# Kernel optimization log

Measured on AMD Instinct MI355X. Metric: run time of the kernel, lower is better.

The kernel has to match this reference:

```python
import jax, jax.numpy as jnp
import numpy as np
from jax import lax

BS = 16; NG = 512; L = 2048; HOP = 512; ZD = 128; HD = 512
FS = L // 2 + 1
TAR = (NG - 1) * HOP + L  # 263680, matches int((NG+3)/4*L)
PPC = 5; PPK = 65
LOG10 = float(np.log(10.0))

def _hann_periodic(n):
    return (0.5 * (1.0 - np.cos(2.0 * np.pi * np.arange(n) / n))).astype(np.float32)

# filter window: fftshift(hann_window(L)) (torch periodic hann)
_FW = jnp.asarray(np.fft.fftshift(_hann_periodic(L)))
# OLA windows with edge correction (first/last grain half set to center value 1.0)
_w = _hann_periodic(L)
_ow = np.tile(_w[None, :], (NG, 1))
_ow[0, : L // 2] = _w[L // 2]
_ow[-1, L // 2 :] = _w[L // 2]
_OLA_W = jnp.asarray(_ow)  # [NG, L]
# overlap-add scatter indices and divisor (fold(unfold(ones)))
_IDX = jnp.asarray((np.arange(NG)[:, None] * HOP + np.arange(L)[None, :]).reshape(-1))
_DIV = jnp.zeros((TAR,), jnp.float32).at[_IDX].add(1.0)


def setup_inputs() -> dict:
    key = jax.random.key(0)
    ks = jax.random.split(key, 8)
    s = 0.02
    d = {}
    d["z"] = jax.random.normal(ks[0], (BS * NG, ZD), jnp.float32)
    d["w0"] = jax.random.normal(ks[1], (ZD, HD), jnp.float32) * s
    d["b0"] = jnp.zeros((HD,), jnp.float32)
    d["g0"] = jnp.ones((HD,), jnp.float32)
    d["be0"] = jnp.zeros((HD,), jnp.float32)
    d["w1"] = jax.random.normal(ks[2], (HD, HD), jnp.float32) * s
    d["b1"] = jnp.zeros((HD,), jnp.float32)
    d["g1"] = jnp.ones((HD,), jnp.float32)
    d["be1"] = jnp.zeros((HD,), jnp.float32)
    d["w2"] = jax.random.normal(ks[3], (HD, HD), jnp.float32) * s
    d["b2"] = jnp.zeros((HD,), jnp.float32)
    d["g2"] = jnp.ones((HD,), jnp.float32)
    d["be2"] = jnp.zeros((HD,), jnp.float32)
    d["w3"] = jax.random.normal(ks[4], (HD, FS), jnp.float32) * s
    d["b3"] = jnp.zeros((FS,), jnp.float32)
    d["pp_w"] = jax.random.normal(ks[5], (1, PPC, PPK), jnp.float32) * s
    d["pp_b"] = jnp.zeros((1,), jnp.float32)
    d["noise"] = jax.random.uniform(ks[6], (BS * NG, L), jnp.float32) * 2.0 - 1.0
    return d


def _lin_bn_lrelu(x, w, b, g, be):
    h = x @ w + b
    m = h.mean(0)
    v = jnp.mean((h - m) ** 2, 0)  # biased var (train-mode BatchNorm1d)
    h = (h - m) * lax.rsqrt(v + 1e-5) * g + be
    return jnp.where(h >= 0, h, 0.2 * h)  # LeakyReLU(0.2)


def reference(z, w0, b0, g0, be0, w1, b1, g1, be1, w2, b2, g2, be2, w3, b3, pp_w, pp_b, noise):
    # decoder MLP -> filter coefficients
    h = _lin_bn_lrelu(z, w0, b0, g0, be0)
    h = _lin_bn_lrelu(h, w1, b1, g1, be1)
    h = _lin_bn_lrelu(h, w2, b2, g2, be2)
    fc = h @ w3 + b3  # [BS*NG, FS]
    fc = 2.0 * jax.nn.sigmoid(fc) ** LOG10 + 1e-7  # mod_sigmoid
    # noise filtering in spectral domain
    ir = jnp.fft.irfft(fc.astype(jnp.complex64), n=L, axis=-1).astype(jnp.float32)
    ir = jnp.fft.fftshift(ir * _FW[None, :], axes=-1)
    audio = jnp.fft.irfft(jnp.fft.rfft(noise, axis=-1) * jnp.fft.rfft(ir, axis=-1), n=L, axis=-1).astype(jnp.float32)
    # per-grain windowing + overlap-add (nn.Fold equivalent scatter-add)
    audio = audio.reshape(BS, NG, L) * _OLA_W[None]
    audio_sum = jnp.zeros((BS, TAR), jnp.float32).at[:, _IDX].add(audio.reshape(BS, -1))
    audio_sum = audio_sum / _DIV  # normalize_ola
    # post-processing conv (PPC replicated channels -> 1) + softsign
    x = jnp.broadcast_to(audio_sum[:, None, :], (BS, PPC, TAR))
    y = lax.conv_general_dilated(x, pp_w, (1,), [(PPK // 2, PPK // 2)], dimension_numbers=("NCH", "OIH", "NCH"))
    y = y[:, 0, :] + pp_b[0]
    return y / (1.0 + jnp.abs(y))
```

## Files before the change

### kernel.cpp

```cpp
#include <hip/hip_runtime.h>
#include <hip/hip_bf16.h>
#include <math.h>

#define TARLEN 263680
#define POWEXP 2.302585092994046f
#define PC(i) ((i) + ((i) >> 3))

typedef __attribute__((ext_vector_type(8))) short bf16x8;
typedef __attribute__((ext_vector_type(8))) ushort u16x8;
typedef __attribute__((ext_vector_type(4))) float f32x4;
typedef __attribute__((ext_vector_type(2))) float pf2;

__device__ __forceinline__ void gload16(const void* g, void* l) {
    __builtin_amdgcn_global_load_lds((const __attribute__((address_space(1))) void*)g,
                                     (__attribute__((address_space(3))) void*)l, 16, 0, 0);
}

__device__ __forceinline__ float bf16f(ushort u) {
    union { uint u; float f; } v; v.u = (uint)u << 16; return v.f;
}
__device__ __forceinline__ ushort fbf16(float x) {
    __hip_bfloat16 h = __float2bfloat16(x);
    return *reinterpret_cast<ushort*>(&h);
}

__device__ __forceinline__ float vsin_rev(float rev) {
    float r; asm("v_sin_f32 %0, %1" : "=v"(r) : "v"(rev)); return r;
}
__device__ __forceinline__ float vcos_rev(float rev) {
    float r; asm("v_cos_f32 %0, %1" : "=v"(r) : "v"(rev)); return r;
}

__device__ __forceinline__ pf2 cmulp(pf2 a, float c, float s) {
    return a * c + a.yx * (pf2){-s, s};
}

__global__ __launch_bounds__(512) void gemm8(
    const ushort* __restrict__ A, const ushort* __restrict__ Bt,
    const float* __restrict__ bias, ushort* __restrict__ C,
    int K, float* __restrict__ ps, float* __restrict__ pq)
{
    __shared__ ushort As[3][4096];
    __shared__ ushort Bs[3][4096];
    __shared__ float sred[8][2][16];
    __shared__ float qred[8][2][16];
    const int tid = threadIdx.x;
    const int lane = tid & 63;
    const int wid = tid >> 6;
    const int nwg = gridDim.x * gridDim.y;
    const int bid = blockIdx.y * gridDim.x + blockIdx.x;
    const int q8 = nwg >> 3;
    const int swzb = (bid & 7) * q8 + (bid >> 3);
    const int bx = swzb % gridDim.x;
    const int by = swzb / gridDim.x;
    const int m0 = by * 128;
    const int n0 = bx * 128;
    const int NT = K >> 5;

    f32x4 acc[4][2];
#pragma unroll
    for (int m = 0; m < 4; ++m)
#pragma unroll
        for (int n = 0; n < 2; ++n)
            acc[m][n] = (f32x4){0.f, 0.f, 0.f, 0.f};

    const int srow = tid >> 2;
    const int scol = (((tid & 3) ^ ((tid >> 3) & 3)) << 3);

    auto stage = [&](int t, int buf) {
        const int k0 = t << 5;
        gload16(A + (size_t)(m0 + srow) * K + k0 + scol, &As[buf][tid * 8]);
        gload16(Bt + (size_t)(n0 + srow) * K + k0 + scol, &Bs[buf][tid * 8]);
    };

    const int lr = lane & 15;
    const int sw8 = (((lane >> 4) ^ ((lane >> 1) & 3)) << 3);
    const int wm0 = (wid >> 2) * 64;
    const int wn0 = (wid & 3) * 32;

    stage(0, 0);
    stage(1, 1);
    for (int t = 0; t < NT; ++t) {
        const int cur = t % 3;
        if (t + 2 < NT) {
            asm volatile("s_waitcnt vmcnt(2)" ::: "memory");
            __builtin_amdgcn_s_barrier();
            stage(t + 2, (t + 2) % 3);
        } else {
            asm volatile("s_waitcnt vmcnt(0)" ::: "memory");
            __builtin_amdgcn_s_barrier();
        }
        const ushort* as = As[cur];
        const ushort* bs = Bs[cur];
        bf16x8 af[4], bfv[2];
#pragma unroll
        for (int m = 0; m < 4; ++m)
            af[m] = *reinterpret_cast<const bf16x8*>(&as[(wm0 + m * 16 + lr) * 32 + sw8]);
#pragma unroll
        for (int n = 0; n < 2; ++n)
            bfv[n] = *reinterpret_cast<const bf16x8*>(&bs[(wn0 + n * 16 + lr) * 32 + sw8]);
#pragma unroll
        for (int m = 0; m < 4; ++m)
#pragma unroll
            for (int n = 0; n < 2; ++n)
                acc[m][n] = __builtin_amdgcn_mfma_f32_16x16x32_bf16(af[m], bfv[n], acc[m][n], 0, 0, 0);
    }
    __syncthreads();

    const int cr = (lane >> 4) << 2;
    const int cc = lane & 15;
    float sacc[2] = {0.f, 0.f}, qacc[2] = {0.f, 0.f};
#pragma unroll
    for (int m = 0; m < 4; ++m) {
#pragma unroll
        for (int n = 0; n < 2; ++n) {
            int gcol = n0 + wn0 + n * 16 + cc;
            float bv = bias[gcol];
            int grow = m0 + wm0 + m * 16 + cr;
#pragma unroll
            for (int j = 0; j < 4; ++j) {
                float v = acc[m][n][j] + bv;
                sacc[n] += v;
                qacc[n] += v * v;
                C[(size_t)(grow + j) * 512 + gcol] = fbf16(v);
            }
        }
    }
#pragma unroll
    for (int n = 0; n < 2; ++n) {
        float s = sacc[n], q = qacc[n];
        s += __shfl_xor(s, 16); q += __shfl_xor(q, 16);
        s += __shfl_xor(s, 32); q += __shfl_xor(q, 32);
        if (lane < 16) { sred[wid][n][lane] = s; qred[wid][n][lane] = q; }
    }
    __syncthreads();
    if (tid < 128) {
        int wn_ = tid >> 5, n_ = (tid >> 4) & 1, cc_ = tid & 15;
        float s = sred[wn_][n_][cc_] + sred[4 + wn_][n_][cc_];
        float q = qred[wn_][n_][cc_] + qred[4 + wn_][n_][cc_];
        int col = n0 + wn_ * 32 + n_ * 16 + cc_;
        ps[(size_t)by * 512 + col] = s;
        pq[(size_t)by * 512 + col] = q;
    }
}

template<int EPI>
__global__ __launch_bounds__(512) void gemm8n(
    const ushort* __restrict__ H, const ushort* __restrict__ Bt,
    const float* __restrict__ bias,
    const float* __restrict__ psIn, const float* __restrict__ pqIn,
    const float* __restrict__ gamma, const float* __restrict__ beta,
    ushort* __restrict__ C, int K, int Nvalid, int ldc,
    float* __restrict__ psOut, float* __restrict__ pqOut)
{
    __shared__ ushort As[3][4096];
    __shared__ ushort Bs[3][4096];
    __shared__ uint sab[512];
    __shared__ float sred[8][2][16];
    __shared__ float qred[8][2][16];
    const int tid = threadIdx.x;
    const int lane = tid & 63;
    const int wid = tid >> 6;
    const int nwg = gridDim.x * gridDim.y;
    const int bid = blockIdx.y * gridDim.x + blockIdx.x;
    const int q8 = nwg >> 3;
    const int swzb = (bid & 7) * q8 + (bid >> 3);
    const int bx = swzb % gridDim.x;
    const int by = swzb / gridDim.x;
    const int m0 = by * 128;
    const int n0 = bx * 128;
    const int NT = K >> 5;

    {
        int c = tid;
        float s = 0.f, q = 0.f;
#pragma unroll 8
        for (int rg = 0; rg < 64; ++rg) { s += psIn[rg * 512 + c]; q += pqIn[rg * 512 + c]; }
        float m = s * (1.f / 8192.f);
        float v = q * (1.f / 8192.f) - m * m;
        float a = rsqrtf(v + 1e-5f) * gamma[c];
        float b = beta[c] - m * a;
        sab[c] = (uint)fbf16(a) | ((uint)fbf16(b) << 16);
    }

    f32x4 acc[4][2];
#pragma unroll
    for (int m = 0; m < 4; ++m)
#pragma unroll
        for (int n = 0; n < 2; ++n)
            acc[m][n] = (f32x4){0.f, 0.f, 0.f, 0.f};

    const int srow = tid >> 2;
    const int scol = (((tid & 3) ^ ((tid >> 3) & 3)) << 3);
    const int lr = lane & 15;
    const int sw8 = (((lane >> 4) ^ ((lane >> 1) & 3)) << 3);
    const int wm0 = (wid >> 2) * 64;
    const int wn0 = (wid & 3) * 32;

    const size_t arow = (size_t)(m0 + srow) * K + scol;
    const size_t brow = (size_t)(n0 + srow) * K + scol;

    auto stageB = [&](int t, int buf) {
        gload16(Bt + brow + (t << 5), &Bs[buf][tid * 8]);
    };
    auto loadA = [&](int t, u16x8& dst) {
        dst = *reinterpret_cast<const u16x8*>(H + arow + (t << 5));
    };

    __syncthreads();

    u16x8 a0, a1;
    stageB(0, 0); loadA(0, a0);
    stageB(1, 1); loadA(1, a1);

    auto iter = [&](int t, u16x8& ar) {
        const int cur = t % 3;
        if (t + 2 < NT) asm volatile("s_waitcnt vmcnt(2)" ::: "memory");
        else            asm volatile("s_waitcnt vmcnt(0)" ::: "memory");
        {
            const uint* pk = &sab[(t << 5) + scol];
            u16x8 o;
#pragma unroll
            for (int j = 0; j < 8; ++j) {
                uint w = pk[j];
                float a = bf16f((ushort)(w & 0xffffu));
                float b = bf16f((ushort)(w >> 16));
                float y = fmaf(bf16f(ar[j]), a, b);
                o[j] = fbf16(y >= 0.f ? y : 0.2f * y);
            }
            *reinterpret_cast<u16x8*>(&As[cur][tid * 8]) = o;
        }
        asm volatile("s_waitcnt lgkmcnt(0)" ::: "memory");
        __builtin_amdgcn_s_barrier();
        if (t + 2 < NT) { stageB(t + 2, (t + 2) % 3); loadA(t + 2, ar); }
        const ushort* as = As[cur];
        const ushort* bs = Bs[cur];
        bf16x8 af[4], bfv[2];
#pragma unroll
        for (int m = 0; m < 4; ++m)
            af[m] = *reinterpret_cast<const bf16x8*>(&as[(wm0 + m * 16 + lr) * 32 + sw8]);
#pragma unroll
        for (int n = 0; n < 2; ++n)
            bfv[n] = *reinterpret_cast<const bf16x8*>(&bs[(wn0 + n * 16 + lr) * 32 + sw8]);
#pragma unroll
        for (int m = 0; m < 4; ++m)
#pragma unroll
            for (int n = 0; n < 2; ++n)
                acc[m][n] = __builtin_amdgcn_mfma_f32_16x16x32_bf16(af[m], bfv[n], acc[m][n], 0, 0, 0);
    };

    for (int t = 0; t < NT; t += 2) { iter(t, a0); iter(t + 1, a1); }
    __syncthreads();

    const int cr = (lane >> 4) << 2;
    const int cc = lane & 15;
    float sacc[2] = {0.f, 0.f}, qacc[2] = {0.f, 0.f};
#pragma unroll
    for (int m = 0; m < 4; ++m) {
#pragma unroll
        for (int n = 0; n < 2; ++n) {
            int gcol = n0 + wn0 + n * 16 + cc;
            if (EPI == 0 || gcol < Nvalid) {
                float bv = bias[gcol];
                int grow = m0 + wm0 + m * 16 + cr;
#pragma unroll
                for (int j = 0; j < 4; ++j) {
                    float v = acc[m][n][j] + bv;
                    if (EPI == 1) {
                        float sg = 1.f / (1.f + __expf(-v));
                        v = 2.f * __expf(POWEXP * __logf(sg)) + 1e-7f;
                    } else {
                        sacc[n] += v;
                        qacc[n] += v * v;
                    }
                    C[(size_t)(grow + j) * ldc + gcol] = fbf16(v);
                }
            }
        }
    }
    if (EPI == 0) {
#pragma unroll
        for (int n = 0; n < 2; ++n) {
            float s = sacc[n], q = qacc[n];
            s += __shfl_xor(s, 16); q += __shfl_xor(q, 16);
            s += __shfl_xor(s, 32); q += __shfl_xor(q, 32);
            if (lane < 16) { sred[wid][n][lane] = s; qred[wid][n][lane] = q; }
        }
        __syncthreads();
        if (tid < 128) {
            int wn_ = tid >> 5, n_ = (tid >> 4) & 1, cc_ = tid & 15;
            float s = sred[wn_][n_][cc_] + sred[4 + wn_][n_][cc_];
            float q = qred[wn_][n_][cc_] + qred[4 + wn_][n_][cc_];
            int col = n0 + wn_ * 32 + n_ * 16 + cc_;
            psOut[(size_t)by * 512 + col] = s;
            pqOut[(size_t)by * 512 + col] = q;
        }
    }
}

__global__ __launch_bounds__(256) void prep_inputs(
    const float* __restrict__ w0, const float* __restrict__ w1,
    const float* __restrict__ w2, const float* __restrict__ w3,
    const float* __restrict__ z,
    ushort* __restrict__ B0, ushort* __restrict__ B1,
    ushort* __restrict__ B2, ushort* __restrict__ B3,
    ushort* __restrict__ A)
{
    if (blockIdx.z == 4) {
        int bid = blockIdx.y * gridDim.x + blockIdx.x;
        if (bid >= 512) return;
        int idx = (bid * 256 + threadIdx.x) << 3;
        float4 a = *reinterpret_cast<const float4*>(&z[idx]);
        float4 b = *reinterpret_cast<const float4*>(&z[idx + 4]);
        float x[8] = {a.x, a.y, a.z, a.w, b.x, b.y, b.z, b.w};
        u16x8 o;
#pragma unroll
        for (int j = 0; j < 8; ++j) o[j] = fbf16(x[j]);
        *reinterpret_cast<u16x8*>(&A[idx]) = o;
        return;
    }
    const float* w; ushort* Bt; int K, N, GX, GY;
    switch (blockIdx.z) {
        case 0: w = w0; Bt = B0; K = 128; N = 512;  GX = 4;  GY = 16; break;
        case 1: w = w1; Bt = B1; K = 512; N = 512;  GX = 16; GY = 16; break;
        case 2: w = w2; Bt = B2; K = 512; N = 512;  GX = 16; GY = 16; break;
        default:w = w3; Bt = B3; K = 512; N = 1025; GX = 16; GY = 36; break;
    }
    if ((int)blockIdx.x >= GX || (int)blockIdx.y >= GY) return;
    __shared__ float tile[32][33];
    int k0 = blockIdx.x * 32, n0 = blockIdx.y * 32;
    int tx = threadIdx.x & 31, ty = threadIdx.x >> 5;
#pragma unroll
    for (int r = 0; r < 4; ++r) {
        int k = k0 + ty + r * 8;
        int n = n0 + tx;
        tile[ty + r * 8][tx] = (n < N) ? w[(size_t)k * N + n] : 0.f;
    }
    __syncthreads();
#pragma unroll
    for (int r = 0; r < 4; ++r) {
        int n = n0 + ty + r * 8;
        int k = k0 + tx;
        Bt[(size_t)n * K + k] = fbf16(tile[tx][ty + r * 8]);
    }
}

template<bool INV, int L>
__device__ __forceinline__ void stk_stage(
    const pf2* __restrict__ s, pf2* __restrict__ d, int t)
{
    int k = t & (L - 1);
    pf2 x0 = s[PC(t)];
    pf2 x1 = s[PC(t + 256)];
    pf2 x2 = s[PC(t + 512)];
    pf2 x3 = s[PC(t + 768)];
    if (L > 1) {
        float rev = (float)k * (1.0f / (float)(4 * L));
        float s1 = vsin_rev(rev), c1 = vcos_rev(rev);
        if (!INV) s1 = -s1;
        float c2 = c1 * c1 - s1 * s1, s2 = 2.f * c1 * s1;
        float c3 = c2 * c1 - s2 * s1, s3 = s2 * c1 + c2 * s1;
        x1 = cmulp(x1, c1, s1);
        x2 = cmulp(x2, c2, s2);
        x3 = cmulp(x3, c3, s3);
    }
    pf2 a = x0 + x2, b = x0 - x2, c = x1 + x3, e = x1 - x3;
    pf2 en = INV ? (pf2){-e.y, e.x} : (pf2){e.y, -e.x};
    int db = ((t - k) << 2) + k;
    d[PC(db)]         = a + c;
    d[PC(db + 2 * L)] = a - c;
    d[PC(db + L)]     = b + en;
    d[PC(db + 3 * L)] = b - en;
}

__global__ __launch_bounds__(256) void fft_filter_kernel(
    const float* __restrict__ noise, const ushort* __restrict__ fcsb,
    ushort* __restrict__ awb)
{
    __shared__ pf2 X[1152], Y[1152];
    __shared__ ushort Fb[1026];
    const int tid = threadIdx.x;
    const int r = blockIdx.x;

    const pf2* nrow = reinterpret_cast<const pf2*>(noise + ((size_t)r << 11));
    for (int i = tid; i < 1025; i += 256) Fb[i] = fcsb[(size_t)r * 1040 + i];
    {
        pf2 x0 = nrow[tid], x1 = nrow[tid + 256], x2 = nrow[tid + 512], x3 = nrow[tid + 768];
        pf2 a = x0 + x2, b = x0 - x2, c = x1 + x3, e = x1 - x3;
        pf2 en = (pf2){e.y, -e.x};
        int db = tid << 2;
        Y[PC(db)]     = a + c;
        Y[PC(db + 1)] = b + en;
        Y[PC(db + 2)] = a - c;
        Y[PC(db + 3)] = b - en;
    }
    __syncthreads();
    stk_stage<false, 4>(Y, X, tid);   __syncthreads();
    stk_stage<false, 16>(X, Y, tid);  __syncthreads();
    stk_stage<false, 64>(Y, X, tid);  __syncthreads();
    stk_stage<false, 256>(X, Y, tid); __syncthreads();

    const float INV1024 = 1.0f / 1024.0f;
    auto proc = [&](int k, float c, float s) {
        int k2 = (1024 - k) & 1023;
        pf2 za = Y[PC(k)], zb = Y[PC(k2)];
        float Fer = 0.5f * (za.x + zb.x), Fei = 0.5f * (za.y - zb.y);
        float For = 0.5f * (za.y + zb.y), Foi = 0.5f * (zb.x - za.x);
        float wFr = c * For - s * Foi;
        float wFi = c * Foi + s * For;
        float Xkr = Fer + wFr, Xki = Fei + wFi;
        float Xbr = Fer - wFr, Xbi = wFi - Fei;
        float Hk, Hb;
        {
            float cl = (k == 0) ? bf16f(Fb[1]) : bf16f(Fb[k - 1]);
            float crr = (k == 1024) ? bf16f(Fb[1023]) : bf16f(Fb[k + 1]);
            float h = 0.5f * bf16f(Fb[k]) + 0.25f * (cl + crr);
            Hk = ((k & 1) ? -h : h) * INV1024;
        }
        {
            int kb = 1024 - k;
            float cl = (kb == 0) ? bf16f(Fb[1]) : bf16f(Fb[kb - 1]);
            float crr = (kb == 1024) ? bf16f(Fb[1023]) : bf16f(Fb[kb + 1]);
            float h = 0.5f * bf16f(Fb[kb]) + 0.25f * (cl + crr);
            Hb = ((kb & 1) ? -h : h) * INV1024;
        }
        float Ykr = Hk * Xkr, Yki = Hk * Xki;
        float Ybr = Hb * Xbr, Ybi = Hb * Xbi;
        if (k == 0) {
            X[PC(0)] = (pf2){0.5f * (Ykr + Ybr), 0.5f * (Ykr - Ybr)};
        } else {
            float Ger = 0.5f * (Ykr + Ybr), Gei = 0.5f * (Yki - Ybi);
            float Sgr = 0.5f * (Ykr - Ybr), Sgi = 0.5f * (Yki + Ybi);
            float wpr = c, wpi = -s;
            float Gor = wpr * Sgr - wpi * Sgi;
            float Goi = wpr * Sgi + wpi * Sgr;
            X[PC(k)]  = (pf2){Ger - Goi, Gei + Gor};
            X[PC(k2)] = (pf2){Ger + Goi, Gor - Gei};
        }
    };
    {
        float rev0 = (float)tid * (1.0f / 2048.0f);
        float c0 = vcos_rev(rev0), s0 = -vsin_rev(rev0);
        proc(tid, c0, s0);
        float rev1 = (float)(tid + 256) * (1.0f / 2048.0f);
        float c1 = vcos_rev(rev1), s1 = -vsin_rev(rev1);
        proc(tid + 256, c1, s1);
        if (tid == 0) proc(512, 0.f, -1.f);
    }
    __syncthreads();

    stk_stage<true, 1>(X, Y, tid);  __syncthreads();
    stk_stage<true, 4>(Y, X, tid);  __syncthreads();
    stk_stage<true, 16>(X, Y, tid); __syncthreads();
    stk_stage<true, 64>(Y, X, tid); __syncthreads();

    {
        const int g = r & 511;
        ushort2* awrow = reinterpret_cast<ushort2*>(awb + ((size_t)r << 11));
        int t = tid;
        pf2 x0 = X[PC(t)], x1 = X[PC(t + 256)], x2 = X[PC(t + 512)], x3 = X[PC(t + 768)];
        float rev = (float)t * (1.0f / 1024.0f);
        float s1 = vsin_rev(rev), c1 = vcos_rev(rev);
        float c2 = c1 * c1 - s1 * s1, s2 = 2.f * c1 * s1;
        float c3 = c2 * c1 - s2 * s1, s3 = s2 * c1 + c2 * s1;
        x1 = cmulp(x1, c1, s1);
        x2 = cmulp(x2, c2, s2);
        x3 = cmulp(x3, c3, s3);
        pf2 a = x0 + x2, b = x0 - x2, c = x1 + x3, e = x1 - x3;
        pf2 en = (pf2){-e.y, e.x};
        pf2 o[4];
        o[0] = a + c;
        o[1] = b + en;
        o[2] = a - c;
        o[3] = b - en;
        float cq[4] = {c1, -s1, -c1, s1};
        float sq[4] = {s1, c1, -s1, -c1};
        const float COSD = 0.99999529380958f;
        const float SIND = 0.00306795676296f;
#pragma unroll
        for (int q = 0; q < 4; ++q) {
            int n = t + 256 * q;
            float w0, w1;
            bool edge = (g == 0 && q < 2) || (g == 511 && q >= 2);
            if (edge) { w0 = 1.f; w1 = 1.f; }
            else {
                w0 = 0.5f - 0.5f * cq[q];
                w1 = 0.5f - 0.5f * (cq[q] * COSD - sq[q] * SIND);
            }
            ushort2 ov; ov.x = fbf16(o[q].x * w0); ov.y = fbf16(o[q].y * w1);
            awrow[n] = ov;
        }
    }
}

__global__ __launch_bounds__(256) void ola_ppconv_kernel(
    const ushort* __restrict__ awb, const float* __restrict__ ppw,
    const float* __restrict__ ppb, float* __restrict__ out)
{
    __shared__ float tile[320];
    __shared__ float Ksh[65];
    int t0 = blockIdx.x * 256;
    int b = blockIdx.y;
    const ushort* awbase = awb + ((size_t)(b * 512) << 11);
    for (int i = threadIdx.x; i < 320; i += 256) {
        int tt = t0 - 32 + i;
        float v = 0.f;
        if (tt >= 1536 && tt < 262144) {
            int glo = (tt - 1536) >> 9;
            const ushort* p = awbase + ((size_t)glo << 11) + (tt - (glo << 9));
            float s = bf16f(p[0]) + bf16f(p[1536]) + bf16f(p[3072]) + bf16f(p[4608]);
            v = s * 0.25f;
        } else if (tt >= 0 && tt < TARLEN) {
            int ghi = min(511, tt >> 9);
            int glo = max(0, (tt - 1536) >> 9);
            float s = 0.f;
            for (int g = glo; g <= ghi; ++g) {
                int n = tt - (g << 9);
                s += bf16f(awbase[((size_t)g << 11) + n]);
            }
            v = s / (float)(ghi - glo + 1);
        }
        tile[i] = v;
    }
    if (threadIdx.x < 65) {
        float k = 0.f;
#pragma unroll
        for (int c = 0; c < 5; ++c) k += ppw[c * 65 + threadIdx.x];
        Ksh[threadIdx.x] = k;
    }
    __syncthreads();
    float y = ppb[0];
#pragma unroll
    for (int j = 0; j < 65; ++j) y = fmaf(Ksh[j], tile[threadIdx.x + j], y);
    int t = t0 + threadIdx.x;
    out[(size_t)b * TARLEN + t] = y / (1.f + fabsf(y));
}

extern "C" void kernel_launch(void* const* d_in, const int* in_sizes, int n_in,
                              void* d_out, int out_size, void* d_ws, size_t ws_size,
                              hipStream_t stream) {
    const float* z    = (const float*)d_in[0];
    const float* w0   = (const float*)d_in[1];
    const float* b0   = (const float*)d_in[2];
    const float* g0   = (const float*)d_in[3];
    const float* be0  = (const float*)d_in[4];
    const float* w1   = (const float*)d_in[5];
    const float* b1   = (const float*)d_in[6];
    const float* g1   = (const float*)d_in[7];
    const float* be1  = (const float*)d_in[8];
    const float* w2   = (const float*)d_in[9];
    const float* b2   = (const float*)d_in[10];
    const float* g2   = (const float*)d_in[11];
    const float* be2  = (const float*)d_in[12];
    const float* w3   = (const float*)d_in[13];
    const float* b3   = (const float*)d_in[14];
    const float* ppw  = (const float*)d_in[15];
    const float* ppb  = (const float*)d_in[16];
    const float* noise= (const float*)d_in[17];
    float* out = (float*)d_out;
    float* ws = (float*)d_ws;

    ushort* h0b = (ushort*)ws;
    ushort* h1b = (ushort*)(ws + 2097152);
    float* ps0  = ws + 4194304;
    float* pq0  = ps0 + 32768;
    float* ps1  = pq0 + 32768;
    float* pq1  = ps1 + 32768;
    float* base = pq1 + 32768;
    ushort* Bt0 = (ushort*)base;
    ushort* Bt1 = (ushort*)(base + 32768);
    ushort* Bt2 = (ushort*)(base + 163840);
    ushort* Bt3 = (ushort*)(base + 294912);
    ushort* fcsb= (ushort*)(base + 589824);
    ushort* awb = (ushort*)(base + 4849664);
    ushort* A   = (ushort*)(base + 13238272);
    ushort* h2b = h0b;

    dim3 blk(256);
    dim3 gblk(512);
    prep_inputs<<<dim3(16, 36, 5), blk, 0, stream>>>(
        w0, w1, w2, w3, z, Bt0, Bt1, Bt2, Bt3, A);
    gemm8<<<dim3(4, 64), gblk, 0, stream>>>(A, Bt0, b0, h0b, 128, ps0, pq0);
    gemm8n<0><<<dim3(4, 64), gblk, 0, stream>>>(
        h0b, Bt1, b1, ps0, pq0, g0, be0, h1b, 512, 512, 512, ps1, pq1);
    gemm8n<0><<<dim3(4, 64), gblk, 0, stream>>>(
        h1b, Bt2, b2, ps1, pq1, g1, be1, h2b, 512, 512, 512, ps0, pq0);
    gemm8n<1><<<dim3(9, 64), gblk, 0, stream>>>(
        h2b, Bt3, b3, ps0, pq0, g2, be2, fcsb, 512, 1025, 1040, nullptr, nullptr);
    fft_filter_kernel<<<dim3(8192), blk, 0, stream>>>(noise, fcsb, awb);
    ola_ppconv_kernel<<<dim3(1030, 16), blk, 0, stream>>>(awb, ppw, ppb, out);
    (void)in_sizes; (void)n_in; (void)out_size; (void)ws_size;
}
```

Measured before the change: 161.7 us.

## Restructure per-row FFT filter into single-wavefront register radix-16 FFT

The FFT filter kernel now runs one 64-lane wavefront per row instead of a 256-thread block. Each lane keeps 16 complex values in registers and runs radix-16 DFTs, with one LDS transpose between passes and a final radix-4 step done across lanes through DPP swizzles. Block-wide __syncthreads are replaced by lgkmcnt waits within the wave, and the padding scheme changes to cut LDS bank conflicts. The cost is higher register pressure and recurrence-based twiddles that may lose some precision. Window values are now computed per element with hardware sin/cos.

```diff
diff --git a/kernel.cpp b/kernel.cpp
--- a/kernel.cpp
+++ b/kernel.cpp
@@ -4,7 +4,7 @@
 
 #define TARLEN 263680
 #define POWEXP 2.302585092994046f
-#define PC(i) ((i) + ((i) >> 3))
+#define S5(k) ((k) + ((k) >> 5))
 
 typedef __attribute__((ext_vector_type(8))) short bf16x8;
 typedef __attribute__((ext_vector_type(8))) ushort u16x8;
@@ -33,6 +33,65 @@
 
 __device__ __forceinline__ pf2 cmulp(pf2 a, float c, float s) {
     return a * c + a.yx * (pf2){-s, s};
+}
+
+__device__ __forceinline__ float dppx1(float x) {
+    return __int_as_float(__builtin_amdgcn_update_dpp(
+        0, __float_as_int(x), 0xB1, 0xF, 0xF, true));
+}
+__device__ __forceinline__ float dppx2(float x) {
+    return __int_as_float(__builtin_amdgcn_update_dpp(
+        0, __float_as_int(x), 0x4E, 0xF, 0xF, true));
+}
+
+#define WAVE_FENCE() asm volatile("s_waitcnt lgkmcnt(0)" ::: "memory")
+
+template<bool INV>
+__device__ __forceinline__ void bf4(pf2& x0, pf2& x1, pf2& x2, pf2& x3) {
+    pf2 a = x0 + x2, b = x0 - x2, cc = x1 + x3, e = x1 - x3;
+    pf2 en = INV ? (pf2){-e.y, e.x} : (pf2){e.y, -e.x};
+    x0 = a + cc; x2 = a - cc; x1 = b + en; x3 = b - en;
+}
+
+__device__ __forceinline__ constexpr int dsw(int k) { return ((k & 3) << 2) | (k >> 2); }
+
+template<bool INV>
+__device__ __forceinline__ void dft16(pf2 v[16]) {
+#pragma unroll
+    for (int a0 = 0; a0 < 4; ++a0)
+        bf4<INV>(v[a0], v[4 + a0], v[8 + a0], v[12 + a0]);
+    const float TC[10] = {1.f, 0.92387953f, 0.70710678f, 0.38268343f, 0.f,
+                          0.f, -0.70710678f, 0.f, 0.f, -0.92387953f};
+    const float TS[10] = {0.f, -0.38268343f, -0.70710678f, -0.92387953f, -1.f,
+                          0.f, -0.70710678f, 0.f, 0.f, 0.38268343f};
+#pragma unroll
+    for (int q0 = 1; q0 < 4; ++q0)
+#pragma unroll
+        for (int a0 = 1; a0 < 4; ++a0) {
+            const int p = a0 * q0;
+            float cx = TC[p];
+            float sx = INV ? -TS[p] : TS[p];
+            v[4 * q0 + a0] = cmulp(v[4 * q0 + a0], cx, sx);
+        }
+#pragma unroll
+    for (int q0 = 0; q0 < 4; ++q0)
+        bf4<INV>(v[4 * q0 + 0], v[4 * q0 + 1], v[4 * q0 + 2], v[4 * q0 + 3]);
+}
+
+template<bool INV>
+__device__ __forceinline__ pf2 xl_radix4(pf2 v, int c) {
+    pf2 t; t.x = dppx2(v.x); t.y = dppx2(v.y);
+    pf2 sum = v + t, dif = t - v;
+    pf2 u = (c & 2) ? dif : sum;
+    pf2 t2; t2.x = dppx1(u.x); t2.y = dppx1(u.y);
+    pf2 res;
+    if (c == 0)      res = u + t2;
+    else if (c == 1) res = t2 - u;
+    else if (c == 2) res = INV ? (pf2){u.x - t2.y, u.y + t2.x}
+                               : (pf2){u.x + t2.y, u.y - t2.x};
+    else             res = INV ? (pf2){t2.x + u.y, t2.y - u.x}
+                               : (pf2){t2.x - u.y, t2.y + u.x};
+    return res;
 }
 
 __global__ __launch_bounds__(512) void gemm8(
@@ -345,150 +404,171 @@
     }
 }
 
-template<bool INV, int L>
-__device__ __forceinline__ void stk_stage(
-    const pf2* __restrict__ s, pf2* __restrict__ d, int t)
-{
-    int k = t & (L - 1);
-    pf2 x0 = s[PC(t)];
-    pf2 x1 = s[PC(t + 256)];
-    pf2 x2 = s[PC(t + 512)];
-    pf2 x3 = s[PC(t + 768)];
-    if (L > 1) {
-        float rev = (float)k * (1.0f / (float)(4 * L));
-        float s1 = vsin_rev(rev), c1 = vcos_rev(rev);
-        if (!INV) s1 = -s1;
-        float c2 = c1 * c1 - s1 * s1, s2 = 2.f * c1 * s1;
-        float c3 = c2 * c1 - s2 * s1, s3 = s2 * c1 + c2 * s1;
-        x1 = cmulp(x1, c1, s1);
-        x2 = cmulp(x2, c2, s2);
-        x3 = cmulp(x3, c3, s3);
-    }
-    pf2 a = x0 + x2, b = x0 - x2, c = x1 + x3, e = x1 - x3;
-    pf2 en = INV ? (pf2){-e.y, e.x} : (pf2){e.y, -e.x};
-    int db = ((t - k) << 2) + k;
-    d[PC(db)]         = a + c;
-    d[PC(db + 2 * L)] = a - c;
-    d[PC(db + L)]     = b + en;
-    d[PC(db + 3 * L)] = b - en;
-}
-
-__global__ __launch_bounds__(256) void fft_filter_kernel(
+__global__ __launch_bounds__(64) void fft_filter_kernel(
     const float* __restrict__ noise, const ushort* __restrict__ fcsb,
     ushort* __restrict__ awb)
 {
-    __shared__ pf2 X[1152], Y[1152];
-    __shared__ ushort Fb[1026];
-    const int tid = threadIdx.x;
-    const int r = blockIdx.x;
-
-    const pf2* nrow = reinterpret_cast<const pf2*>(noise + ((size_t)r << 11));
-    for (int i = tid; i < 1025; i += 256) Fb[i] = fcsb[(size_t)r * 1040 + i];
+    __shared__ pf2 E[1056];
+    __shared__ ushort F[1026];
+    const int l = threadIdx.x;
+    const int row = blockIdx.x;
+    const int c = l & 3;
+    const int k0 = l >> 2;
+    const int rc = ((c & 1) << 1) | (c >> 1);
+
+    const ushort* frow = fcsb + (size_t)row * 1040;
+#pragma unroll
+    for (int j = 0; j < 16; ++j) F[l + (j << 6)] = frow[l + (j << 6)];
+    if (l == 0) F[1024] = frow[1024];
+
+    pf2 v[16];
     {
-        pf2 x0 = nrow[tid], x1 = nrow[tid + 256], x2 = nrow[tid + 512], x3 = nrow[tid + 768];
-        pf2 a = x0 + x2, b = x0 - x2, c = x1 + x3, e = x1 - x3;
-        pf2 en = (pf2){e.y, -e.x};
-        int db = tid << 2;
-        Y[PC(db)]     = a + c;
-        Y[PC(db + 1)] = b + en;
-        Y[PC(db + 2)] = a - c;
-        Y[PC(db + 3)] = b - en;
-    }
-    __syncthreads();
-    stk_stage<false, 4>(Y, X, tid);   __syncthreads();
-    stk_stage<false, 16>(X, Y, tid);  __syncthreads();
-    stk_stage<false, 64>(Y, X, tid);  __syncthreads();
-    stk_stage<false, 256>(X, Y, tid); __syncthreads();
-
-    const float INV1024 = 1.0f / 1024.0f;
-    auto proc = [&](int k, float c, float s) {
-        int k2 = (1024 - k) & 1023;
-        pf2 za = Y[PC(k)], zb = Y[PC(k2)];
-        float Fer = 0.5f * (za.x + zb.x), Fei = 0.5f * (za.y - zb.y);
-        float For = 0.5f * (za.y + zb.y), Foi = 0.5f * (zb.x - za.x);
-        float wFr = c * For - s * Foi;
-        float wFi = c * Foi + s * For;
-        float Xkr = Fer + wFr, Xki = Fei + wFi;
-        float Xbr = Fer - wFr, Xbi = wFi - Fei;
-        float Hk, Hb;
+        const pf2* nrow = reinterpret_cast<const pf2*>(noise + ((size_t)row << 11));
+#pragma unroll
+        for (int a = 0; a < 16; ++a) v[a] = nrow[(a << 6) + l];
+        dft16<false>(v);
         {
-            float cl = (k == 0) ? bf16f(Fb[1]) : bf16f(Fb[k - 1]);
-            float crr = (k == 1024) ? bf16f(Fb[1023]) : bf16f(Fb[k + 1]);
-            float h = 0.5f * bf16f(Fb[k]) + 0.25f * (cl + crr);
-            Hk = ((k & 1) ? -h : h) * INV1024;
-        }
+            float rev = (float)(l >> 2) * (1.f / 256.f);
+            float wc = vcos_rev(rev), ws = -vsin_rev(rev);
+            float tc = wc, ts = ws;
+            v[dsw(1)] = cmulp(v[dsw(1)], tc, ts);
+#pragma unroll
+            for (int k = 2; k < 16; ++k) {
+                float ntc = tc * wc - ts * ws;
+                ts = tc * ws + ts * wc; tc = ntc;
+                v[dsw(k)] = cmulp(v[dsw(k)], tc, ts);
+            }
+        }
+#pragma unroll
+        for (int k = 0; k < 16; ++k) E[k * 66 + l] = v[dsw(k)];
+        WAVE_FENCE();
+#pragma unroll
+        for (int b = 0; b < 16; ++b) v[b] = E[k0 * 66 + (b << 2) + c];
+        dft16<false>(v);
         {
-            int kb = 1024 - k;
-            float cl = (kb == 0) ? bf16f(Fb[1]) : bf16f(Fb[kb - 1]);
-            float crr = (kb == 1024) ? bf16f(Fb[1023]) : bf16f(Fb[kb + 1]);
-            float h = 0.5f * bf16f(Fb[kb]) + 0.25f * (cl + crr);
-            Hb = ((kb & 1) ? -h : h) * INV1024;
-        }
-        float Ykr = Hk * Xkr, Yki = Hk * Xki;
-        float Ybr = Hb * Xbr, Ybi = Hb * Xbi;
-        if (k == 0) {
-            X[PC(0)] = (pf2){0.5f * (Ykr + Ybr), 0.5f * (Ykr - Ybr)};
-        } else {
-            float Ger = 0.5f * (Ykr + Ybr), Gei = 0.5f * (Yki - Ybi);
-            float Sgr = 0.5f * (Ykr - Ybr), Sgi = 0.5f * (Yki + Ybi);
-            float wpr = c, wpi = -s;
-            float Gor = wpr * Sgr - wpi * Sgi;
-            float Goi = wpr * Sgi + wpi * Sgr;
-            X[PC(k)]  = (pf2){Ger - Goi, Gei + Gor};
-            X[PC(k2)] = (pf2){Ger + Goi, Gor - Gei};
-        }
-    };
+            float rev0 = (float)(c * k0) * (1.f / 1024.f);
+            float tc = vcos_rev(rev0), ts = -vsin_rev(rev0);
+            float revs = (float)c * (1.f / 64.f);
+            float wc = vcos_rev(revs), ws = -vsin_rev(revs);
+            v[dsw(0)] = cmulp(v[dsw(0)], tc, ts);
+#pragma unroll
+            for (int k = 1; k < 16; ++k) {
+                float ntc = tc * wc - ts * ws;
+                ts = tc * ws + ts * wc; tc = ntc;
+                v[dsw(k)] = cmulp(v[dsw(k)], tc, ts);
+            }
+        }
+        WAVE_FENCE();
+#pragma unroll
+        for (int k1 = 0; k1 < 16; ++k1) {
+            pf2 res = xl_radix4<false>(v[dsw(k1)], c);
+            E[S5(k0 + (k1 << 4) + (rc << 8))] = res;
+        }
+    }
+    WAVE_FENCE();
     {
-        float rev0 = (float)tid * (1.0f / 2048.0f);
-        float c0 = vcos_rev(rev0), s0 = -vsin_rev(rev0);
-        proc(tid, c0, s0);
-        float rev1 = (float)(tid + 256) * (1.0f / 2048.0f);
-        float c1 = vcos_rev(rev1), s1 = -vsin_rev(rev1);
-        proc(tid + 256, c1, s1);
-        if (tid == 0) proc(512, 0.f, -1.f);
-    }
-    __syncthreads();
-
-    stk_stage<true, 1>(X, Y, tid);  __syncthreads();
-    stk_stage<true, 4>(Y, X, tid);  __syncthreads();
-    stk_stage<true, 16>(X, Y, tid); __syncthreads();
-    stk_stage<true, 64>(Y, X, tid); __syncthreads();
-
+        const float INV1024 = 1.0f / 1024.0f;
+        auto procfn = [&](int k, float pc, float ps) {
+            int k2 = (1024 - k) & 1023;
+            pf2 za = E[S5(k)], zb = E[S5(k2)];
+            float Fer = 0.5f * (za.x + zb.x), Fei = 0.5f * (za.y - zb.y);
+            float For = 0.5f * (za.y + zb.y), Foi = 0.5f * (zb.x - za.x);
+            float wFr = pc * For - ps * Foi;
+            float wFi = pc * Foi + ps * For;
+            float Xkr = Fer + wFr, Xki = Fei + wFi;
+            float Xbr = Fer - wFr, Xbi = wFi - Fei;
+            float Hk, Hb;
+            {
+                float cl = (k == 0) ? bf16f(F[1]) : bf16f(F[k - 1]);
+                float crr = bf16f(F[k + 1]);
+                float h = 0.5f * bf16f(F[k]) + 0.25f * (cl + crr);
+                Hk = ((k & 1) ? -h : h) * INV1024;
+            }
+            {
+                int kb = 1024 - k;
+                float cl = bf16f(F[kb - 1]);
+                float crr = (kb == 1024) ? bf16f(F[1023]) : bf16f(F[kb + 1]);
+                float h = 0.5f * bf16f(F[kb]) + 0.25f * (cl + crr);
+                Hb = ((kb & 1) ? -h : h) * INV1024;
+            }
+            float Ykr = Hk * Xkr, Yki = Hk * Xki;
+            float Ybr = Hb * Xbr, Ybi = Hb * Xbi;
+            if (k == 0) {
+                E[S5(0)] = (pf2){0.5f * (Ykr + Ybr), 0.5f * (Ykr - Ybr)};
+            } else {
+                float Ger = 0.5f * (Ykr + Ybr), Gei = 0.5f * (Yki - Ybi);
+                float Sgr = 0.5f * (Ykr - Ybr), Sgi = 0.5f * (Yki + Ybi);
+                float wpr = pc, wpi = -ps;
+                float Gor = wpr * Sgr - wpi * Sgi;
+                float Goi = wpr * Sgi + wpi * Sgr;
+                E[S5(k)]  = (pf2){Ger - Goi, Gei + Gor};
+                E[S5(k2)] = (pf2){Ger + Goi, Gor - Gei};
+            }
+        };
+#pragma unroll
+        for (int j = 0; j < 8; ++j) {
+            int k = l + (j << 6);
+            float rev = (float)k * (1.f / 2048.f);
+            procfn(k, vcos_rev(rev), -vsin_rev(rev));
+        }
+        if (l == 0) procfn(512, 0.f, -1.f);
+    }
+    WAVE_FENCE();
     {
-        const int g = r & 511;
-        ushort2* awrow = reinterpret_cast<ushort2*>(awb + ((size_t)r << 11));
-        int t = tid;
-        pf2 x0 = X[PC(t)], x1 = X[PC(t + 256)], x2 = X[PC(t + 512)], x3 = X[PC(t + 768)];
-        float rev = (float)t * (1.0f / 1024.0f);
-        float s1 = vsin_rev(rev), c1 = vcos_rev(rev);
-        float c2 = c1 * c1 - s1 * s1, s2 = 2.f * c1 * s1;
-        float c3 = c2 * c1 - s2 * s1, s3 = s2 * c1 + c2 * s1;
-        x1 = cmulp(x1, c1, s1);
-        x2 = cmulp(x2, c2, s2);
-        x3 = cmulp(x3, c3, s3);
-        pf2 a = x0 + x2, b = x0 - x2, c = x1 + x3, e = x1 - x3;
-        pf2 en = (pf2){-e.y, e.x};
-        pf2 o[4];
-        o[0] = a + c;
-        o[1] = b + en;
-        o[2] = a - c;
-        o[3] = b - en;
-        float cq[4] = {c1, -s1, -c1, s1};
-        float sq[4] = {s1, c1, -s1, -c1};
+#pragma unroll
+        for (int a = 0; a < 16; ++a) v[a] = E[S5((a << 6) + l)];
+        dft16<true>(v);
+        {
+            float rev = (float)(l >> 2) * (1.f / 256.f);
+            float wc = vcos_rev(rev), ws = vsin_rev(rev);
+            float tc = wc, ts = ws;
+            v[dsw(1)] = cmulp(v[dsw(1)], tc, ts);
+#pragma unroll
+            for (int k = 2; k < 16; ++k) {
+                float ntc = tc * wc - ts * ws;
+                ts = tc * ws + ts * wc; tc = ntc;
+                v[dsw(k)] = cmulp(v[dsw(k)], tc, ts);
+            }
+        }
+        WAVE_FENCE();
+#pragma unroll
+        for (int k = 0; k < 16; ++k) E[k * 66 + l] = v[dsw(k)];
+        WAVE_FENCE();
+#pragma unroll
+        for (int b = 0; b < 16; ++b) v[b] = E[k0 * 66 + (b << 2) + c];
+        dft16<true>(v);
+        {
+            float rev0 = (float)(c * k0) * (1.f / 1024.f);
+            float tc = vcos_rev(rev0), ts = vsin_rev(rev0);
+            float revs = (float)c * (1.f / 64.f);
+            float wc = vcos_rev(revs), ws = vsin_rev(revs);
+            v[dsw(0)] = cmulp(v[dsw(0)], tc, ts);
+#pragma unroll
+            for (int k = 1; k < 16; ++k) {
+                float ntc = tc * wc - ts * ws;
+                ts = tc * ws + ts * wc; tc = ntc;
+                v[dsw(k)] = cmulp(v[dsw(k)], tc, ts);
+            }
+        }
+        const int g = row & 511;
+        ushort2* awrow = reinterpret_cast<ushort2*>(awb + ((size_t)row << 11));
         const float COSD = 0.99999529380958f;
         const float SIND = 0.00306795676296f;
 #pragma unroll
-        for (int q = 0; q < 4; ++q) {
-            int n = t + 256 * q;
+        for (int k1 = 0; k1 < 16; ++k1) {
+            pf2 res = xl_radix4<true>(v[dsw(k1)], c);
+            int i = k0 + (k1 << 4) + (rc << 8);
             float w0, w1;
-            bool edge = (g == 0 && q < 2) || (g == 511 && q >= 2);
+            bool edge = (g == 0 && i < 512) || (g == 511 && i >= 512);
             if (edge) { w0 = 1.f; w1 = 1.f; }
             else {
-                w0 = 0.5f - 0.5f * cq[q];
-                w1 = 0.5f - 0.5f * (cq[q] * COSD - sq[q] * SIND);
-            }
-            ushort2 ov; ov.x = fbf16(o[q].x * w0); ov.y = fbf16(o[q].y * w1);
-            awrow[n] = ov;
+                float rev = (float)i * (1.f / 1024.f);
+                float ci = vcos_rev(rev), si = vsin_rev(rev);
+                w0 = 0.5f - 0.5f * ci;
+                w1 = 0.5f - 0.5f * (ci * COSD - si * SIND);
+            }
+            ushort2 ov; ov.x = fbf16(res.x * w0); ov.y = fbf16(res.y * w1);
+            awrow[i] = ov;
         }
     }
 }
@@ -587,7 +667,7 @@
         h1b, Bt2, b2, ps1, pq1, g1, be1, h2b, 512, 512, 512, ps0, pq0);
     gemm8n<1><<<dim3(9, 64), gblk, 0, stream>>>(
         h2b, Bt3, b3, ps0, pq0, g2, be2, fcsb, 512, 1025, 1040, nullptr, nullptr);
-    fft_filter_kernel<<<dim3(8192), blk, 0, stream>>>(noise, fcsb, awb);
+    fft_filter_kernel<<<dim3(8192), dim3(64), 0, stream>>>(noise, fcsb, awb);
     ola_ppconv_kernel<<<dim3(1030, 16), blk, 0, stream>>>(awb, ppw, ppb, out);
     (void)in_sizes; (void)n_in; (void)out_size; (void)ws_size;
 }
```

Result: slower. 166.8 us (+3.2%).
